# Kernel tuning notes

Measured on AMD Instinct MI355X. Metric: run time of the kernel, lower is better.

The kernel has to match this reference:

```python
import jax, jax.numpy as jnp
import numpy as np

BATCH = 16384
N_FEAT = 2048
SWAP_PROB = 0.1


def setup_inputs() -> dict:
    key = jax.random.key(0)
    k_x, k_mask, k_perm = jax.random.split(key, 3)
    x = jax.random.normal(k_x, (BATCH, N_FEAT), dtype=jnp.float32)
    # swap_mask[i, j] = True with prob swap_prob (matches torch.rand(...) < swap_prob)
    swap_mask = jax.random.uniform(k_mask, (BATCH, N_FEAT)) < SWAP_PROB
    # per-row random permutation (matches torch.randperm per batch row),
    # vectorized as argsort of iid uniforms
    perm = jnp.argsort(jax.random.uniform(k_perm, (BATCH, N_FEAT)), axis=1).astype(jnp.int32)
    return {"x": x, "swap_mask": swap_mask, "perm": perm}


def reference(x, swap_mask, perm):
    # x[i, swap_mask[i]] = x[i, perm[i][swap_mask[i]]]  (vectorized over rows)
    swapped = jnp.take_along_axis(x, perm, axis=1)  # [B, F]
    return jnp.where(swap_mask, swapped, x)
```

## Files before the change

kernel.cpp:

```cpp
#include <hip/hip_runtime.h>

#define NFEAT 2048
#define BATCH 16384

__global__ __launch_bounds__(256) void swap_corrupt_kernel(
    const float* __restrict__ x,
    const int*   __restrict__ mask,
    const int*   __restrict__ perm,
    float*       __restrict__ out)
{
    __shared__ float row[NFEAT];

    const int r = blockIdx.x;
    const int t = threadIdx.x;
    const size_t base = (size_t)r * NFEAT;

    const float4* __restrict__ x4 = (const float4*)(x + base);
    float4 a = x4[t];
    float4 b = x4[t + 256];
    ((float4*)row)[t]       = a;
    ((float4*)row)[t + 256] = b;
    __syncthreads();

    const int4* __restrict__ m4 = (const int4*)(mask + base);
    const int4* __restrict__ p4 = (const int4*)(perm + base);
    float4* __restrict__ o4 = (float4*)(out + base);

    {
        int4 m = m4[t];
        int4 p = p4[t];
        float4 o;
        o.x = m.x ? row[p.x] : a.x;
        o.y = m.y ? row[p.y] : a.y;
        o.z = m.z ? row[p.z] : a.z;
        o.w = m.w ? row[p.w] : a.w;
        o4[t] = o;
    }
    {
        int4 m = m4[t + 256];
        int4 p = p4[t + 256];
        float4 o;
        o.x = m.x ? row[p.x] : b.x;
        o.y = m.y ? row[p.y] : b.y;
        o.z = m.z ? row[p.z] : b.z;
        o.w = m.w ? row[p.w] : b.w;
        o4[t + 256] = o;
    }
}

extern "C" void kernel_launch(void* const* d_in, const int* in_sizes, int n_in,
                              void* d_out, int out_size, void* d_ws, size_t ws_size,
                              hipStream_t stream) {
    const float* x    = (const float*)d_in[0];
    const int*   mask = (const int*)d_in[1];
    const int*   perm = (const int*)d_in[2];
    float*       out  = (float*)d_out;

    swap_corrupt_kernel<<<dim3(BATCH), dim3(256), 0, stream>>>(x, mask, perm, out);
}
```

Baseline: 380.8 us.

## Gather directly from global memory and process multiple rows per block

Removes the shared-memory row staging and the barrier, so each element is read from global memory with the index picked by the mask (the permuted index or its own column). Each block now handles eight rows in a loop, and the grid shrinks to match. The aim is to drop LDS traffic and synchronisation and to amortise block launch cost. In exchange, x is no longer loaded as float4: every element becomes a scalar global load, partly random, which relies on L2 hits for the row and may lose coalescing efficiency.

New measurement: 401.5 us. 5.4% more time.

```diff
diff --git a/kernel.cpp b/kernel.cpp
--- a/kernel.cpp
+++ b/kernel.cpp
@@ -2,6 +2,8 @@
 
 #define NFEAT 2048
 #define BATCH 16384
+#define ROWS_PER_BLOCK 8
+#define NBLOCKS (BATCH / ROWS_PER_BLOCK)
 
 __global__ __launch_bounds__(256) void swap_corrupt_kernel(
     const float* __restrict__ x,
@@ -9,42 +11,40 @@
     const int*   __restrict__ perm,
     float*       __restrict__ out)
 {
-    __shared__ float row[NFEAT];
+    const int t = threadIdx.x;
 
-    const int r = blockIdx.x;
-    const int t = threadIdx.x;
-    const size_t base = (size_t)r * NFEAT;
+    #pragma unroll 2
+    for (int rr = 0; rr < ROWS_PER_BLOCK; ++rr) {
+        const int r = blockIdx.x * ROWS_PER_BLOCK + rr;
+        const size_t base = (size_t)r * NFEAT;
 
-    const float4* __restrict__ x4 = (const float4*)(x + base);
-    float4 a = x4[t];
-    float4 b = x4[t + 256];
-    ((float4*)row)[t]       = a;
-    ((float4*)row)[t + 256] = b;
-    __syncthreads();
+        const float* __restrict__ xr = x + base;
+        const int4*  __restrict__ m4 = (const int4*)(mask + base);
+        const int4*  __restrict__ p4 = (const int4*)(perm + base);
+        float4*      __restrict__ o4 = (float4*)(out + base);
 
-    const int4* __restrict__ m4 = (const int4*)(mask + base);
-    const int4* __restrict__ p4 = (const int4*)(perm + base);
-    float4* __restrict__ o4 = (float4*)(out + base);
-
-    {
-        int4 m = m4[t];
-        int4 p = p4[t];
-        float4 o;
-        o.x = m.x ? row[p.x] : a.x;
-        o.y = m.y ? row[p.y] : a.y;
-        o.z = m.z ? row[p.z] : a.z;
-        o.w = m.w ? row[p.w] : a.w;
-        o4[t] = o;
-    }
-    {
-        int4 m = m4[t + 256];
-        int4 p = p4[t + 256];
-        float4 o;
-        o.x = m.x ? row[p.x] : b.x;
-        o.y = m.y ? row[p.y] : b.y;
-        o.z = m.z ? row[p.z] : b.z;
-        o.w = m.w ? row[p.w] : b.w;
-        o4[t + 256] = o;
+        {
+            int4 m = m4[t];
+            int4 p = p4[t];
+            const int c0 = 4 * t;
+            float4 o;
+            o.x = xr[m.x ? p.x : c0];
+            o.y = xr[m.y ? p.y : c0 + 1];
+            o.z = xr[m.z ? p.z : c0 + 2];
+            o.w = xr[m.w ? p.w : c0 + 3];
+            o4[t] = o;
+        }
+        {
+            int4 m = m4[t + 256];
+            int4 p = p4[t + 256];
+            const int c0 = 4 * (t + 256);
+            float4 o;
+            o.x = xr[m.x ? p.x : c0];
+            o.y = xr[m.y ? p.y : c0 + 1];
+            o.z = xr[m.z ? p.z : c0 + 2];
+            o.w = xr[m.w ? p.w : c0 + 3];
+            o4[t + 256] = o;
+        }
     }
 }
 
@@ -56,5 +56,5 @@
     const int*   perm = (const int*)d_in[2];
     float*       out  = (float*)d_out;
 
-    swap_corrupt_kernel<<<dim3(BATCH), dim3(256), 0, stream>>>(x, mask, perm, out);
+    swap_corrupt_kernel<<<dim3(NBLOCKS), dim3(256), 0, stream>>>(x, mask, perm, out);
 }
```
